# Performance work log

Hardware: AMD Instinct MI355X
Metric: run time of the kernel (lower is better)

## Reference

```python
import jax, jax.numpy as jnp
import numpy as np

DIM = 768
NUM_HEADS = 12
HEAD_DIM = DIM // NUM_HEADS
GRID = 32  # H == W
EPS = 1e-6


def setup_inputs() -> dict:
    key = jax.random.key(0)
    ks = jax.random.split(key, 8)
    B, N = 8, GRID * GRID
    x = jax.random.normal(ks[0], (B, N, DIM), dtype=jnp.float32)
    policy = jax.random.randint(ks[1], (B, N, 1), 0, 2).astype(jnp.float32)
    qkv_w = jax.random.normal(ks[2], (3 * DIM, DIM), dtype=jnp.float32) * 0.02
    qkv_b = jax.random.normal(ks[3], (3 * DIM,), dtype=jnp.float32) * 0.02
    proj_w = jax.random.normal(ks[4], (DIM, DIM), dtype=jnp.float32) * 0.02
    proj_b = jax.random.normal(ks[5], (DIM,), dtype=jnp.float32) * 0.02
    rel_pos_h = jax.random.normal(ks[6], (2 * GRID - 1, HEAD_DIM), dtype=jnp.float32) * 0.02
    rel_pos_w = jax.random.normal(ks[7], (2 * GRID - 1, HEAD_DIM), dtype=jnp.float32) * 0.02
    return {"x": x, "policy": policy, "qkv_w": qkv_w, "qkv_b": qkv_b,
            "proj_w": proj_w, "proj_b": proj_b,
            "rel_pos_h": rel_pos_h, "rel_pos_w": rel_pos_w, "H": GRID, "W": GRID}


def _attention(x, policy, qkv_w, qkv_b, proj_w, proj_b, rel_pos_h, rel_pos_w, H, W):
    B, N, C = x.shape
    nh, hd = NUM_HEADS, C // NUM_HEADS
    scale = hd ** (-0.5)
    # qkv projection: [B,N,3C] -> [3, B*nh, N, hd]
    qkv = (x @ qkv_w.T + qkv_b).reshape(B, N, 3, nh, hd)
    qkv = qkv.transpose(2, 0, 3, 1, 4).reshape(3, B * nh, N, hd)
    q, k, v = qkv[0], qkv[1], qkv[2]
    attn = jnp.einsum("bqd,bkd->bqk", q * scale, k)  # [B*nh, N, N]
    # decomposed relative position bias (q_size == k_size == (H, W))
    coords = jnp.arange(H)
    Rh = rel_pos_h[coords[:, None] - coords[None, :] + (H - 1)]  # [H,H,hd]
    coords_w = jnp.arange(W)
    Rw = rel_pos_w[coords_w[:, None] - coords_w[None, :] + (W - 1)]  # [W,W,hd]
    r_q = q.reshape(B * nh, H, W, hd)
    rel_h = jnp.einsum("bhwc,hkc->bhwk", r_q, Rh)  # [B*nh,H,W,H]
    rel_w = jnp.einsum("bhwc,wkc->bhwk", r_q, Rw)  # [B*nh,H,W,W]
    attn = (attn.reshape(B * nh, H, W, H, W)
            + rel_h[:, :, :, :, None]
            + rel_w[:, :, :, None, :]).reshape(B * nh, N, N)
    # policy-masked softmax
    attn = attn.reshape(B, nh, N, N)
    ap = policy.reshape(B, 1, 1, N)
    ap = ap + (1.0 - ap) * jnp.eye(N, dtype=ap.dtype)  # always attend to self
    max_att = jnp.max(attn, axis=-1, keepdims=True)
    e = jnp.exp(attn - max_att).astype(jnp.float32) * ap.astype(jnp.float32)
    attn = ((e + EPS / N) / (jnp.sum(e, axis=-1, keepdims=True) + EPS)).astype(x.dtype)
    out = jnp.einsum("bqk,bkd->bqd", attn.reshape(B * nh, N, N), v)
    out = out.reshape(B, nh, N, hd).transpose(0, 2, 1, 3).reshape(B, N, C)
    return out @ proj_w.T + proj_b


def reference(x, policy, qkv_w, qkv_b, proj_w, proj_b, rel_pos_h, rel_pos_w, H, W):
    return _attention(x, policy, qkv_w, qkv_b, proj_w, proj_b, rel_pos_h, rel_pos_w, H, W)
```

## Files before the change

kernel.cpp:

```cpp
#include <hip/hip_runtime.h>
#include <hip/hip_bf16.h>

#define B_   8
#define N_   1024
#define C_   768
#define NH_  12
#define HD_  64
#define BH_  96
#define EPS_ 1e-6f
#define EPSN_ (1e-6f / 1024.0f)
#define SQ_  0.1803368801111244f

typedef __bf16 bf16;
typedef __attribute__((ext_vector_type(8))) __bf16  bf16x8;
typedef __attribute__((ext_vector_type(4))) __bf16  bf16x4;
typedef __attribute__((ext_vector_type(4))) float   floatx4;

#define MFMA16(a, b, c) __builtin_amdgcn_mfma_f32_16x16x32_bf16((a), (b), (c), 0, 0, 0)

__device__ __forceinline__ void gld16(const void* g, void* l) {
  typedef unsigned int u32;
  __builtin_amdgcn_global_load_lds(
      (const __attribute__((address_space(1))) u32*)g,
      (__attribute__((address_space(3))) u32*)l, 16, 0, 0);
}
__device__ __forceinline__ float bfu2f(unsigned int u) {
  union { unsigned int i; float f; } v; v.i = u << 16; return v.f;
}
__device__ __forceinline__ float bfhi2f(unsigned int u) {
  union { unsigned int i; float f; } v; v.i = u & 0xffff0000u; return v.f;
}
__device__ __forceinline__ unsigned short f2bfu(float f) {
  union { float f; unsigned int i; } v; v.f = f;
  return (unsigned short)((v.i + 0x7FFFu + ((v.i >> 16) & 1u)) >> 16);
}

__global__ __launch_bounds__(256) void prep_kernel(
    const float* __restrict__ x, const float* __restrict__ qkv_w,
    const float* __restrict__ proj_w, const float* __restrict__ relh,
    const float* __restrict__ relw,
    bf16* __restrict__ Xb, bf16* __restrict__ Wq, bf16* __restrict__ Wp,
    bf16* __restrict__ Rhb, bf16* __restrict__ Rwb) {
  int bid = blockIdx.x;
  if (bid < 8448) {
    const float* in; bf16* out; int i;
    if (bid < 6144)      { in = x;      out = Xb; i = bid * 256 + threadIdx.x; }
    else if (bid < 7872) { in = qkv_w;  out = Wq; i = (bid - 6144) * 256 + threadIdx.x; }
    else                 { in = proj_w; out = Wp; i = (bid - 7872) * 256 + threadIdx.x; }
    float4 v = ((const float4*)in)[i];
    bf16x4 o = {(bf16)v.x, (bf16)v.y, (bf16)v.z, (bf16)v.w};
    ((bf16x4*)out)[i] = o;
  } else {
    const float* in = (bid < 8464) ? relh : relw;
    bf16* out = (bid < 8464) ? Rhb : Rwb;
    int i = ((bid < 8464) ? (bid - 8448) : (bid - 8464)) * 256 + threadIdx.x;
    int r = i >> 6;
    out[i] = (r < 63) ? (bf16)(in[i] * 8.0f) : (bf16)0.0f;
  }
}

__global__ __launch_bounds__(256) void gemm_qkv(
    const bf16* __restrict__ X, const bf16* __restrict__ W,
    const float* __restrict__ bias,
    bf16* __restrict__ Qb, bf16* __restrict__ Kb, bf16* __restrict__ Vb) {
  __shared__ __align__(16) bf16 As[2][8192];
  __shared__ __align__(16) bf16 Bs[2][8192];
  const int tid = threadIdx.x;
  const int lane = tid & 63, quad = lane >> 4, c16 = lane & 15;
  const int wid = tid >> 6;
  const int wm = (wid >> 1) * 64, wn = (wid & 1) * 64;
  const int m0 = blockIdx.x * 128, n0 = blockIdx.y * 128;
  const bool flip = (blockIdx.y < 12);
  floatx4 acc[4][4];
#pragma unroll
  for (int i = 0; i < 4; ++i)
#pragma unroll
    for (int j = 0; j < 4; ++j) acc[i][j] = {0.f, 0.f, 0.f, 0.f};

  auto stage = [&](int k0, int buf) {
#pragma unroll
    for (int t = 0; t < 4; ++t) {
      int task = t * 256 + tid;
      int r = task >> 3, lg = (task & 7) ^ (r & 7);
      int wbase = (t * 256 + (tid & 192)) * 8;
      gld16(X + (size_t)(m0 + r) * 768 + k0 + lg * 8, &As[buf][wbase]);
      gld16(W + (size_t)(n0 + r) * 768 + k0 + lg * 8, &Bs[buf][wbase]);
    }
  };

  stage(0, 0);
  for (int it = 0; it < 12; ++it) {
    const int cur = it & 1;
    __syncthreads();
    if (it < 11) stage((it + 1) * 64, cur ^ 1);
#pragma unroll
    for (int kw = 0; kw < 2; ++kw) {
      bf16x8 af[4], bfr[4];
#pragma unroll
      for (int i = 0; i < 4; ++i) {
        int r = wm + i * 16 + c16, pg = (kw * 4 + quad) ^ (c16 & 7);
        af[i] = *(bf16x8*)&As[cur][r * 64 + pg * 8];
      }
#pragma unroll
      for (int j = 0; j < 4; ++j) {
        int r = wn + j * 16 + c16, pg = (kw * 4 + quad) ^ (c16 & 7);
        bfr[j] = *(bf16x8*)&Bs[cur][r * 64 + pg * 8];
      }
      if (flip) {
#pragma unroll
        for (int a = 0; a < 4; ++a)
#pragma unroll
          for (int b = 0; b < 4; ++b) acc[a][b] = MFMA16(bfr[a], af[b], acc[a][b]);
      } else {
#pragma unroll
        for (int i = 0; i < 4; ++i)
#pragma unroll
          for (int j = 0; j < 4; ++j) acc[i][j] = MFMA16(af[i], bfr[j], acc[i][j]);
      }
    }
  }
  if (flip) {
    const bool isQ = (blockIdx.y < 6);
    bf16* base = isQ ? Qb : Kb;
    const int off = isQ ? 0 : 768;
#pragma unroll
    for (int a = 0; a < 4; ++a) {
      int jb = n0 + wn + a * 16 + quad * 4;
      float4 b4 = *(const float4*)&bias[jb];
      int head = (jb - off) >> 6;
      int d = jb & 63;
#pragma unroll
      for (int b = 0; b < 4; ++b) {
        int tok = m0 + wm + b * 16 + c16;
        int bb = tok >> 10, n = tok & 1023;
        float v0 = acc[a][b][0] + b4.x, v1 = acc[a][b][1] + b4.y;
        float v2 = acc[a][b][2] + b4.z, v3 = acc[a][b][3] + b4.w;
        if (isQ) { v0 *= SQ_; v1 *= SQ_; v2 *= SQ_; v3 *= SQ_; }
        bf16x4 o = {(bf16)v0, (bf16)v1, (bf16)v2, (bf16)v3};
        *(bf16x4*)&base[(((size_t)bb * NH_ + head) * N_ + n) * HD_ + d] = o;
      }
    }
  } else {
#pragma unroll
    for (int jt = 0; jt < 4; ++jt) {
      int j = n0 + wn + jt * 16 + c16;
      float bj = bias[j];
      int rem = j - 1536, head = rem >> 6, d = rem & 63;
#pragma unroll
      for (int it = 0; it < 4; ++it) {
        int mbase = m0 + wm + it * 16 + quad * 4;
        int bb = mbase >> 10, n = mbase & 1023;
        bf16x4 o = {(bf16)(acc[it][jt][0] + bj), (bf16)(acc[it][jt][1] + bj),
                    (bf16)(acc[it][jt][2] + bj), (bf16)(acc[it][jt][3] + bj)};
        *(bf16x4*)&Vb[(((size_t)bb * NH_ + head) * HD_ + d) * N_ + n] = o;
      }
    }
  }
}

__global__ __launch_bounds__(256) void vsum_kernel(const bf16* __restrict__ Vb,
                                                   float* __restrict__ Vsum) {
  const int bh = blockIdx.x;
  const int d = threadIdx.x >> 2, part = threadIdx.x & 3;
  const bf16* Vg = Vb + (size_t)bh * (N_ * HD_) + d * N_ + part * 256;
  float s = 0.f;
  for (int i = 0; i < 32; ++i) {
    bf16x8 v = *(const bf16x8*)(Vg + i * 8);
#pragma unroll
    for (int e = 0; e < 8; ++e) s += (float)v[e];
  }
  __shared__ float red[64][4];
  red[d][part] = s;
  __syncthreads();
  if (part == 0) Vsum[bh * 64 + d] = red[d][0] + red[d][1] + red[d][2] + red[d][3];
}

__global__ __launch_bounds__(256, 4) void attn_mfma(
    const bf16* __restrict__ Qb, const bf16* __restrict__ Kb,
    const bf16* __restrict__ Vb, const float* __restrict__ policy,
    const bf16* __restrict__ Rh, const bf16* __restrict__ Rw,
    const float* __restrict__ Vsum, bf16* __restrict__ AO) {
  const int bh = blockIdx.x, qt = blockIdx.y;
  const int b = bh / NH_, head = bh % NH_;
  __shared__ __align__(16) bf16 Qs[4096];
  __shared__ __align__(16) bf16 Ks[4096];
  __shared__ __align__(16) bf16 Vt[4096];
  __shared__ unsigned short RHb[64][34];
  __shared__ unsigned short RWb[64][34];
  __shared__ float polf[1024];
  const int tid = threadIdx.x;
  const int wid = tid >> 6, lane = tid & 63, quad = lane >> 4, c16 = lane & 15;
  const int sw = c16 & 7;
  bf16* Ptw = Qs + wid * 1024;
  const floatx4 zero4 = {0.f, 0.f, 0.f, 0.f};

  const bf16* Qg = Qb + ((size_t)bh * N_ + qt * 64) * HD_;
  const bf16* Kg = Kb + (size_t)bh * (N_ * HD_);
  const bf16* Vg = Vb + (size_t)bh * (N_ * HD_);

#pragma unroll
  for (int t = 0; t < 2; ++t) {
    int task = t * 256 + tid;
    int r = task >> 3, lg = (task & 7) ^ (r & 7);
    int wbase = (t * 256 + (tid & 192)) * 8;
    gld16(Qg + r * 64 + lg * 8, &Qs[wbase]);
    gld16(Rh + r * 64 + lg * 8, &Ks[wbase]);
  }
  gld16(policy + (size_t)b * N_ + tid * 4, &polf[(tid & 192) * 4]);
  __syncthreads();

  bf16x8 aq0 = *(bf16x8*)&Qs[(wid * 16 + c16) * 64 + (quad ^ sw) * 8];
  bf16x8 aq1 = *(bf16x8*)&Qs[(wid * 16 + c16) * 64 + ((4 + quad) ^ sw) * 8];

  {
    floatx4 racc[4];
#pragma unroll
    for (int nt = 0; nt < 4; ++nt) {
      int r = nt * 16 + c16;
      bf16x8 b0 = *(bf16x8*)&Ks[r * 64 + (quad ^ sw) * 8];
      bf16x8 b1 = *(bf16x8*)&Ks[r * 64 + ((4 + quad) ^ sw) * 8];
      racc[nt] = MFMA16(aq1, b1, MFMA16(aq0, b0, zero4));
    }
#pragma unroll
    for (int nt = 0; nt < 4; ++nt)
#pragma unroll
      for (int reg = 0; reg < 4; ++reg) {
        int rloc = wid * 16 + quad * 4 + reg;
        int hh = 2 * qt + (rloc >> 5);
        int krow = hh + 31 - (nt * 16 + c16);
        if ((unsigned)krow < 32u) RHb[rloc][krow] = f2bfu(racc[nt][reg]);
      }
  }
  __syncthreads();
#pragma unroll
  for (int t = 0; t < 2; ++t) {
    int task = t * 256 + tid;
    int r = task >> 3, lg = (task & 7) ^ (r & 7);
    gld16(Rw + r * 64 + lg * 8, &Ks[(t * 256 + (tid & 192)) * 8]);
  }
  __syncthreads();
  {
    floatx4 racc[4];
#pragma unroll
    for (int nt = 0; nt < 4; ++nt) {
      int r = nt * 16 + c16;
      bf16x8 b0 = *(bf16x8*)&Ks[r * 64 + (quad ^ sw) * 8];
      bf16x8 b1 = *(bf16x8*)&Ks[r * 64 + ((4 + quad) ^ sw) * 8];
      racc[nt] = MFMA16(aq1, b1, MFMA16(aq0, b0, zero4));
    }
#pragma unroll
    for (int nt = 0; nt < 4; ++nt)
#pragma unroll
      for (int reg = 0; reg < 4; ++reg) {
        int rloc = wid * 16 + quad * 4 + reg;
        int kcol = (rloc & 31) + 31 - (nt * 16 + c16);
        if ((unsigned)kcol < 32u) RWb[rloc][kcol] = f2bfu(racc[nt][reg]);
      }
  }

  float rwv0[4], rwv1[4];
#pragma unroll
  for (int reg = 0; reg < 4; ++reg) {
    int rloc = wid * 16 + quad * 4 + reg;
    rwv0[reg] = bfu2f(RWb[rloc][c16]);
    rwv1[reg] = bfu2f(RWb[rloc][16 + c16]);
  }
  int ptoff[4][4];
#pragma unroll
  for (int reg = 0; reg < 4; ++reg) {
    int prow = quad * 4 + reg;
#pragma unroll
    for (int nt = 0; nt < 4; ++nt)
      ptoff[reg][nt] = prow * 64 + (c16 & 7) +
                       (((nt * 2 + (c16 >> 3)) ^ (prow & 7)) << 3);
  }

  float l_part[4] = {0.f, 0.f, 0.f, 0.f};
  floatx4 o_acc[4];
#pragma unroll
  for (int i = 0; i < 4; ++i) o_acc[i] = zero4;
  int nqr[4];
#pragma unroll
  for (int reg = 0; reg < 4; ++reg) nqr[reg] = qt * 64 + wid * 16 + quad * 4 + reg;

  for (int kt = 0; kt < 16; ++kt) {
    __syncthreads();
#pragma unroll
    for (int t = 0; t < 2; ++t) {
      int task = t * 256 + tid;
      int r = task >> 3, lg = (task & 7) ^ (r & 7);
      int wbase = (t * 256 + (tid & 192)) * 8;
      gld16(Kg + (size_t)(kt * 64 + r) * 64 + lg * 8, &Ks[wbase]);
      gld16(Vg + (size_t)r * N_ + kt * 64 + lg * 8, &Vt[wbase]);
    }

    floatx4 init[4];
#pragma unroll
    for (int reg = 0; reg < 4; ++reg) {
      int rloc = wid * 16 + quad * 4 + reg;
      unsigned int rhp = *(const unsigned int*)&RHb[rloc][kt * 2];
      float rh0 = bfu2f(rhp & 0xffffu), rh1 = bfhi2f(rhp);
      init[0][reg] = rh0 + rwv0[reg];
      init[1][reg] = rh0 + rwv1[reg];
      init[2][reg] = rh1 + rwv0[reg];
      init[3][reg] = rh1 + rwv1[reg];
    }
    float pm[4];
#pragma unroll
    for (int nt = 0; nt < 4; ++nt) pm[nt] = polf[kt * 64 + nt * 16 + c16];
    __syncthreads();

    floatx4 s[4];
#pragma unroll
    for (int nt = 0; nt < 4; ++nt) {
      int r = nt * 16 + c16;
      bf16x8 bk0 = *(bf16x8*)&Ks[r * 64 + (quad ^ sw) * 8];
      bf16x8 bk1 = *(bf16x8*)&Ks[r * 64 + ((4 + quad) ^ sw) * 8];
      s[nt] = MFMA16(aq1, bk1, MFMA16(aq0, bk0, init[nt]));
    }

#pragma unroll
    for (int reg = 0; reg < 4; ++reg) {
      if (kt != qt) {
#pragma unroll
        for (int nt = 0; nt < 4; ++nt) {
          float e = exp2f(s[nt][reg]) * pm[nt];
          l_part[reg] += e;
          Ptw[ptoff[reg][nt]] = (bf16)e;
        }
      } else {
        const int nq = nqr[reg];
#pragma unroll
        for (int nt = 0; nt < 4; ++nt) {
          int kg = kt * 64 + nt * 16 + c16;
          float mask = (kg == nq) ? 1.f : pm[nt];
          float e = exp2f(s[nt][reg]) * mask;
          l_part[reg] += e;
          Ptw[ptoff[reg][nt]] = (bf16)e;
        }
      }
    }

#pragma unroll
    for (int kw2 = 0; kw2 < 2; ++kw2) {
      bf16x8 ap = *(bf16x8*)&Ptw[c16 * 64 + ((kw2 * 4 + quad) ^ sw) * 8];
#pragma unroll
      for (int dt = 0; dt < 4; ++dt) {
        int r = dt * 16 + c16;
        bf16x8 bv = *(bf16x8*)&Vt[r * 64 + ((kw2 * 4 + quad) ^ sw) * 8];
        o_acc[dt] = MFMA16(ap, bv, o_acc[dt]);
      }
    }
  }

  float inv[4];
#pragma unroll
  for (int reg = 0; reg < 4; ++reg) {
    float l = l_part[reg];
#pragma unroll
    for (int d = 1; d < 16; d <<= 1) l += __shfl_xor(l, d, 64);
    inv[reg] = 1.f / (l + EPS_);
  }
#pragma unroll
  for (int dt = 0; dt < 4; ++dt) {
    int d = dt * 16 + c16;
    float vs = Vsum[bh * 64 + d];
#pragma unroll
    for (int reg = 0; reg < 4; ++reg) {
      float o = (o_acc[dt][reg] + EPSN_ * vs) * inv[reg];
      AO[((size_t)b * N_ + nqr[reg]) * C_ + head * HD_ + d] = (bf16)o;
    }
  }
}

__global__ __launch_bounds__(256) void gemm_proj(
    const bf16* __restrict__ A, const bf16* __restrict__ W,
    const float* __restrict__ bias, float* __restrict__ Out) {
  __shared__ __align__(16) bf16 As[2][8192];
  __shared__ __align__(16) bf16 Bs[2][8192];
  const int tid = threadIdx.x;
  const int lane = tid & 63, quad = lane >> 4, c16 = lane & 15;
  const int wid = tid >> 6;
  const int wm = (wid >> 1) * 64, wn = (wid & 1) * 64;
  const int m0 = blockIdx.x * 128, n0 = blockIdx.y * 128;
  floatx4 acc[4][4];
#pragma unroll
  for (int i = 0; i < 4; ++i)
#pragma unroll
    for (int j = 0; j < 4; ++j) acc[i][j] = {0.f, 0.f, 0.f, 0.f};

  auto stage = [&](int k0, int buf) {
#pragma unroll
    for (int t = 0; t < 4; ++t) {
      int task = t * 256 + tid;
      int r = task >> 3, lg = (task & 7) ^ (r & 7);
      int wbase = (t * 256 + (tid & 192)) * 8;
      gld16(A + (size_t)(m0 + r) * 768 + k0 + lg * 8, &As[buf][wbase]);
      gld16(W + (size_t)(n0 + r) * 768 + k0 + lg * 8, &Bs[buf][wbase]);
    }
  };

  stage(0, 0);
  for (int it = 0; it < 12; ++it) {
    const int cur = it & 1;
    __syncthreads();
    if (it < 11) stage((it + 1) * 64, cur ^ 1);
#pragma unroll
    for (int kw = 0; kw < 2; ++kw) {
      bf16x8 af[4], bfr[4];
#pragma unroll
      for (int i = 0; i < 4; ++i) {
        int r = wm + i * 16 + c16, pg = (kw * 4 + quad) ^ (c16 & 7);
        af[i] = *(bf16x8*)&As[cur][r * 64 + pg * 8];
      }
#pragma unroll
      for (int j = 0; j < 4; ++j) {
        int r = wn + j * 16 + c16, pg = (kw * 4 + quad) ^ (c16 & 7);
        bfr[j] = *(bf16x8*)&Bs[cur][r * 64 + pg * 8];
      }
#pragma unroll
      for (int a = 0; a < 4; ++a)
#pragma unroll
        for (int b = 0; b < 4; ++b) acc[a][b] = MFMA16(bfr[a], af[b], acc[a][b]);
    }
  }
#pragma unroll
  for (int a = 0; a < 4; ++a) {
    int jb = n0 + wn + a * 16 + quad * 4;
    float4 b4 = *(const float4*)&bias[jb];
#pragma unroll
    for (int b = 0; b < 4; ++b) {
      int m = m0 + wm + b * 16 + c16;
      float4 o = make_float4(acc[a][b][0] + b4.x, acc[a][b][1] + b4.y,
                             acc[a][b][2] + b4.z, acc[a][b][3] + b4.w);
      *(float4*)&Out[(size_t)m * 768 + jb] = o;
    }
  }
}

extern "C" void kernel_launch(void* const* d_in, const int* in_sizes, int n_in,
                              void* d_out, int out_size, void* d_ws, size_t ws_size,
                              hipStream_t stream) {
  const float* x      = (const float*)d_in[0];
  const float* policy = (const float*)d_in[1];
  const float* qkv_w  = (const float*)d_in[2];
  const float* qkv_b  = (const float*)d_in[3];
  const float* proj_w = (const float*)d_in[4];
  const float* proj_b = (const float*)d_in[5];
  const float* relh   = (const float*)d_in[6];
  const float* relw   = (const float*)d_in[7];

  char* ws = (char*)d_ws;
  bf16* Xbf   = (bf16*)(ws);
  bf16* Wqkv  = (bf16*)(ws + 12582912);
  bf16* Wproj = (bf16*)(ws + 16121856);
  bf16* Rhb   = (bf16*)(ws + 17301504);
  bf16* Rwb   = (bf16*)(ws + 17309696);
  bf16* Qb    = (bf16*)(ws + 17317888);
  bf16* Kb    = (bf16*)(ws + 29900800);
  bf16* Vb    = (bf16*)(ws + 42483712);
  bf16* AOb   = (bf16*)(ws + 55066624);
  float* Vsum = (float*)(ws + 67649536);

  prep_kernel<<<8480, 256, 0, stream>>>(x, qkv_w, proj_w, relh, relw,
                                        Xbf, Wqkv, Wproj, Rhb, Rwb);
  gemm_qkv<<<dim3(64, 18), 256, 0, stream>>>(Xbf, Wqkv, qkv_b, Qb, Kb, Vb);
  vsum_kernel<<<BH_, 256, 0, stream>>>(Vb, Vsum);
  attn_mfma<<<dim3(BH_, 16), 256, 0, stream>>>(Qb, Kb, Vb, policy, Rhb, Rwb,
                                               Vsum, AOb);
  gemm_proj<<<dim3(64, 6), 256, 0, stream>>>(AOb, Wproj, proj_b, (float*)d_out);
}
```

Baseline: 226.2 us.

## Double-buffer K/V tiles and fold policy mask into additive score bias

K and V tiles are now double-buffered in LDS. The next tile's global-to-LDS load is issued before the current tile is computed, so one barrier per iteration goes away and load latency can overlap the MFMA work. The policy mask is turned once into an additive bias (0 or a large negative value) and added to the score accumulator init, with the diagonal self-attend handled there too. This removes the per-element multiply and the kt==qt branch in the exp loop. The extra LDS lowers the occupancy hint from 4 to 3 blocks per CU, which trades some latency hiding for the prefetch.

```diff
diff --git a/kernel.cpp b/kernel.cpp
--- a/kernel.cpp
+++ b/kernel.cpp
@@ -10,6 +10,7 @@
 #define EPS_ 1e-6f
 #define EPSN_ (1e-6f / 1024.0f)
 #define SQ_  0.1803368801111244f
+#define MNEG_ (-3.0e38f)
 
 typedef __bf16 bf16;
 typedef __attribute__((ext_vector_type(8))) __bf16  bf16x8;
@@ -175,7 +176,7 @@
   if (part == 0) Vsum[bh * 64 + d] = red[d][0] + red[d][1] + red[d][2] + red[d][3];
 }
 
-__global__ __launch_bounds__(256, 4) void attn_mfma(
+__global__ __launch_bounds__(256, 3) void attn_mfma(
     const bf16* __restrict__ Qb, const bf16* __restrict__ Kb,
     const bf16* __restrict__ Vb, const float* __restrict__ policy,
     const bf16* __restrict__ Rh, const bf16* __restrict__ Rw,
@@ -183,11 +184,11 @@
   const int bh = blockIdx.x, qt = blockIdx.y;
   const int b = bh / NH_, head = bh % NH_;
   __shared__ __align__(16) bf16 Qs[4096];
-  __shared__ __align__(16) bf16 Ks[4096];
-  __shared__ __align__(16) bf16 Vt[4096];
+  __shared__ __align__(16) bf16 Ks[2][4096];
+  __shared__ __align__(16) bf16 Vt[2][4096];
   __shared__ unsigned short RHb[64][34];
   __shared__ unsigned short RWb[64][34];
-  __shared__ float polf[1024];
+  __shared__ __align__(16) float polf[1024];
   const int tid = threadIdx.x;
   const int wid = tid >> 6, lane = tid & 63, quad = lane >> 4, c16 = lane & 15;
   const int sw = c16 & 7;
@@ -198,17 +199,37 @@
   const bf16* Kg = Kb + (size_t)bh * (N_ * HD_);
   const bf16* Vg = Vb + (size_t)bh * (N_ * HD_);
 
+  auto stageKV = [&](int kt2, int buf) {
+#pragma unroll
+    for (int t = 0; t < 2; ++t) {
+      int task = t * 256 + tid;
+      int r = task >> 3, lg = (task & 7) ^ (r & 7);
+      int wbase = (t * 256 + (tid & 192)) * 8;
+      gld16(Kg + (size_t)(kt2 * 64 + r) * 64 + lg * 8, &Ks[buf][wbase]);
+      gld16(Vg + (size_t)r * N_ + kt2 * 64 + lg * 8, &Vt[buf][wbase]);
+    }
+  };
+
 #pragma unroll
   for (int t = 0; t < 2; ++t) {
     int task = t * 256 + tid;
     int r = task >> 3, lg = (task & 7) ^ (r & 7);
     int wbase = (t * 256 + (tid & 192)) * 8;
     gld16(Qg + r * 64 + lg * 8, &Qs[wbase]);
-    gld16(Rh + r * 64 + lg * 8, &Ks[wbase]);
+    gld16(Rh + r * 64 + lg * 8, &Ks[0][wbase]);
   }
   gld16(policy + (size_t)b * N_ + tid * 4, &polf[(tid & 192) * 4]);
   __syncthreads();
 
+  stageKV(0, 1);
+
+  {
+    float4 p4 = *(float4*)&polf[tid * 4];
+    float4 m4 = make_float4((p4.x != 0.f) ? 0.f : MNEG_, (p4.y != 0.f) ? 0.f : MNEG_,
+                            (p4.z != 0.f) ? 0.f : MNEG_, (p4.w != 0.f) ? 0.f : MNEG_);
+    *(float4*)&polf[tid * 4] = m4;
+  }
+
   bf16x8 aq0 = *(bf16x8*)&Qs[(wid * 16 + c16) * 64 + (quad ^ sw) * 8];
   bf16x8 aq1 = *(bf16x8*)&Qs[(wid * 16 + c16) * 64 + ((4 + quad) ^ sw) * 8];
 
@@ -217,8 +238,8 @@
 #pragma unroll
     for (int nt = 0; nt < 4; ++nt) {
       int r = nt * 16 + c16;
-      bf16x8 b0 = *(bf16x8*)&Ks[r * 64 + (quad ^ sw) * 8];
-      bf16x8 b1 = *(bf16x8*)&Ks[r * 64 + ((4 + quad) ^ sw) * 8];
+      bf16x8 b0 = *(bf16x8*)&Ks[0][r * 64 + (quad ^ sw) * 8];
+      bf16x8 b1 = *(bf16x8*)&Ks[0][r * 64 + ((4 + quad) ^ sw) * 8];
       racc[nt] = MFMA16(aq1, b1, MFMA16(aq0, b0, zero4));
     }
 #pragma unroll
@@ -236,7 +257,7 @@
   for (int t = 0; t < 2; ++t) {
     int task = t * 256 + tid;
     int r = task >> 3, lg = (task & 7) ^ (r & 7);
-    gld16(Rw + r * 64 + lg * 8, &Ks[(t * 256 + (tid & 192)) * 8]);
+    gld16(Rw + r * 64 + lg * 8, &Ks[0][(t * 256 + (tid & 192)) * 8]);
   }
   __syncthreads();
   {
@@ -244,8 +265,8 @@
 #pragma unroll
     for (int nt = 0; nt < 4; ++nt) {
       int r = nt * 16 + c16;
-      bf16x8 b0 = *(bf16x8*)&Ks[r * 64 + (quad ^ sw) * 8];
-      bf16x8 b1 = *(bf16x8*)&Ks[r * 64 + ((4 + quad) ^ sw) * 8];
+      bf16x8 b0 = *(bf16x8*)&Ks[0][r * 64 + (quad ^ sw) * 8];
+      bf16x8 b1 = *(bf16x8*)&Ks[0][r * 64 + ((4 + quad) ^ sw) * 8];
       racc[nt] = MFMA16(aq1, b1, MFMA16(aq0, b0, zero4));
     }
 #pragma unroll
@@ -284,60 +305,47 @@
   for (int reg = 0; reg < 4; ++reg) nqr[reg] = qt * 64 + wid * 16 + quad * 4 + reg;
 
   for (int kt = 0; kt < 16; ++kt) {
+    const int cur = (kt + 1) & 1;
     __syncthreads();
-#pragma unroll
-    for (int t = 0; t < 2; ++t) {
-      int task = t * 256 + tid;
-      int r = task >> 3, lg = (task & 7) ^ (r & 7);
-      int wbase = (t * 256 + (tid & 192)) * 8;
-      gld16(Kg + (size_t)(kt * 64 + r) * 64 + lg * 8, &Ks[wbase]);
-      gld16(Vg + (size_t)r * N_ + kt * 64 + lg * 8, &Vt[wbase]);
-    }
+    if (kt < 15) stageKV(kt + 1, kt & 1);
 
     floatx4 init[4];
+    float mv0 = polf[kt * 64 + c16],      mv1 = polf[kt * 64 + 16 + c16];
+    float mv2 = polf[kt * 64 + 32 + c16], mv3 = polf[kt * 64 + 48 + c16];
 #pragma unroll
     for (int reg = 0; reg < 4; ++reg) {
       int rloc = wid * 16 + quad * 4 + reg;
       unsigned int rhp = *(const unsigned int*)&RHb[rloc][kt * 2];
       float rh0 = bfu2f(rhp & 0xffffu), rh1 = bfhi2f(rhp);
-      init[0][reg] = rh0 + rwv0[reg];
-      init[1][reg] = rh0 + rwv1[reg];
-      init[2][reg] = rh1 + rwv0[reg];
-      init[3][reg] = rh1 + rwv1[reg];
-    }
-    float pm[4];
-#pragma unroll
-    for (int nt = 0; nt < 4; ++nt) pm[nt] = polf[kt * 64 + nt * 16 + c16];
-    __syncthreads();
+      float m0 = mv0, m1 = mv1, m2 = mv2, m3 = mv3;
+      if (kt == qt && c16 == quad * 4 + reg) {
+        if (wid == 0) m0 = 0.f;
+        else if (wid == 1) m1 = 0.f;
+        else if (wid == 2) m2 = 0.f;
+        else m3 = 0.f;
+      }
+      init[0][reg] = rh0 + rwv0[reg] + m0;
+      init[1][reg] = rh0 + rwv1[reg] + m1;
+      init[2][reg] = rh1 + rwv0[reg] + m2;
+      init[3][reg] = rh1 + rwv1[reg] + m3;
+    }
 
     floatx4 s[4];
 #pragma unroll
     for (int nt = 0; nt < 4; ++nt) {
       int r = nt * 16 + c16;
-      bf16x8 bk0 = *(bf16x8*)&Ks[r * 64 + (quad ^ sw) * 8];
-      bf16x8 bk1 = *(bf16x8*)&Ks[r * 64 + ((4 + quad) ^ sw) * 8];
+      bf16x8 bk0 = *(bf16x8*)&Ks[cur][r * 64 + (quad ^ sw) * 8];
+      bf16x8 bk1 = *(bf16x8*)&Ks[cur][r * 64 + ((4 + quad) ^ sw) * 8];
       s[nt] = MFMA16(aq1, bk1, MFMA16(aq0, bk0, init[nt]));
     }
 
 #pragma unroll
     for (int reg = 0; reg < 4; ++reg) {
-      if (kt != qt) {
-#pragma unroll
-        for (int nt = 0; nt < 4; ++nt) {
-          float e = exp2f(s[nt][reg]) * pm[nt];
-          l_part[reg] += e;
-          Ptw[ptoff[reg][nt]] = (bf16)e;
-        }
-      } else {
-        const int nq = nqr[reg];
-#pragma unroll
-        for (int nt = 0; nt < 4; ++nt) {
-          int kg = kt * 64 + nt * 16 + c16;
-          float mask = (kg == nq) ? 1.f : pm[nt];
-          float e = exp2f(s[nt][reg]) * mask;
-          l_part[reg] += e;
-          Ptw[ptoff[reg][nt]] = (bf16)e;
-        }
+#pragma unroll
+      for (int nt = 0; nt < 4; ++nt) {
+        float e = exp2f(s[nt][reg]);
+        l_part[reg] += e;
+        Ptw[ptoff[reg][nt]] = (bf16)e;
       }
     }
 
@@ -347,7 +355,7 @@
 #pragma unroll
       for (int dt = 0; dt < 4; ++dt) {
         int r = dt * 16 + c16;
-        bf16x8 bv = *(bf16x8*)&Vt[r * 64 + ((kw2 * 4 + quad) ^ sw) * 8];
+        bf16x8 bv = *(bf16x8*)&Vt[cur][r * 64 + ((kw2 * 4 + quad) ^ sw) * 8];
         o_acc[dt] = MFMA16(ap, bv, o_acc[dt]);
       }
     }
```

After: 230.3 us. No clear change (+1.8%).
